# Performance work log

Measured on AMD Instinct MI355X. Metric: run time of the kernel, lower is better.

The kernel has to match this reference:

```python
import jax, jax.numpy as jnp
import numpy as np

N = 8192
F_IN = 512
F_OUT = 64
ALPHA = 0.2  # LeakyReLU negative slope
NEG_INF = -9e15


def setup_inputs() -> dict:
    key = jax.random.key(0)
    k1, k2, k3, k4 = jax.random.split(key, 4)
    inp = jax.random.normal(k1, (N, F_IN), dtype=jnp.float32)
    adj = jax.random.randint(k2, (N, N), 0, 2, dtype=jnp.int32)
    W = jax.random.normal(k3, (F_IN, F_OUT), dtype=jnp.float32) * 0.05
    a = jax.random.normal(k4, (2 * F_OUT, 1), dtype=jnp.float32) * 0.05
    return {"inp": inp, "adj": adj, "W": W, "a": a}


def reference(inp, adj, W, a):
    # h = W(inp): [N, F_OUT]
    h = inp @ W
    # a([h_i || h_j]) decomposes exactly into a1.h_i + a2.h_j, avoiding the
    # [N*N, 2F] concat tensor while computing identical math.
    f1 = h @ a[:F_OUT]        # [N, 1] source-node term
    f2 = h @ a[F_OUT:]        # [N, 1] target-node term
    e = jax.nn.leaky_relu(f1 + f2.T, negative_slope=ALPHA)  # [N, N]
    masked = jnp.where(adj > 0, e, jnp.float32(NEG_INF))
    attention = jax.nn.softmax(masked, axis=1)  # dropout is no-op at inference
    h_prime = attention @ h   # [N, F_OUT]
    return jax.nn.elu(h_prime)  # concat=True branch
```

## Files before the change

kernel.cpp:

```cpp
#include <hip/hip_runtime.h>

#define NN   8192
#define FIN  512
#define FOUT 64

typedef __attribute__((ext_vector_type(8))) short short8;
typedef __attribute__((ext_vector_type(4))) float floatx4;

__device__ __forceinline__ unsigned f2bf_u(float f) {
  union { float f; unsigned u; } v; v.f = f;
  return (v.u + 0x7fffu + ((v.u >> 16) & 1u)) >> 16;
}
__device__ __forceinline__ unsigned pack2(float a, float b) {
  return f2bf_u(a) | (f2bf_u(b) << 16);
}

__global__ __launch_bounds__(256) void k1_gemm_h(
    const float* __restrict__ inp, const float* __restrict__ W,
    const float* __restrict__ a,
    float* __restrict__ f1, float* __restrict__ f2,
    unsigned short* __restrict__ hT)
{
  __shared__ unsigned short at[32][72];
  __shared__ unsigned short wt[64][72];
  __shared__ float hsm[32][65];
  __shared__ float alds[2 * FOUT];

  const int tid   = threadIdx.x;
  const int rbase = blockIdx.x * 32;
  if (tid < 2 * FOUT) alds[tid] = a[tid];

  const int lane = tid & 63;
  const int wv   = tid >> 6;
  const int l15  = lane & 15;
  const int q    = lane >> 4;
  const int mi   = wv & 1;
  const int ni0  = (wv >> 1) * 2;

  const int r_a  = tid >> 3;
  const int k8   = (tid & 7) * 8;
  const int n_w  = tid & 63;
  const int kb_w = (tid >> 6) * 16;

  floatx4 acc0 = {0.f, 0.f, 0.f, 0.f};
  floatx4 acc1 = {0.f, 0.f, 0.f, 0.f};

  for (int kk0 = 0; kk0 < FIN; kk0 += 64) {
    __syncthreads();
    const float* ap = inp + (rbase + r_a) * FIN + kk0 + k8;
    float4 v0 = *(const float4*)ap;
    float4 v1 = *(const float4*)(ap + 4);
    *(uint4*)&at[r_a][k8] = make_uint4(pack2(v0.x, v0.y), pack2(v0.z, v0.w),
                                       pack2(v1.x, v1.y), pack2(v1.z, v1.w));
#pragma unroll
    for (int kk2 = 0; kk2 < 16; ++kk2)
      wt[n_w][kb_w + kk2] = (unsigned short)f2bf_u(W[(kk0 + kb_w + kk2) * FOUT + n_w]);
    __syncthreads();
#pragma unroll
    for (int ks = 0; ks < 2; ++ks) {
      short8 af = *(const short8*)&at[mi * 16 + l15][ks * 32 + q * 8];
      short8 b0 = *(const short8*)&wt[ni0 * 16 + l15][ks * 32 + q * 8];
      short8 b1 = *(const short8*)&wt[(ni0 + 1) * 16 + l15][ks * 32 + q * 8];
      acc0 = __builtin_amdgcn_mfma_f32_16x16x32_bf16(af, b0, acc0, 0, 0, 0);
      acc1 = __builtin_amdgcn_mfma_f32_16x16x32_bf16(af, b1, acc1, 0, 0, 0);
    }
  }

  {
    const int m0 = mi * 16 + q * 4;
    const int i0 = rbase + m0;
    {
      const int n = ni0 * 16 + l15;
#pragma unroll
      for (int rg = 0; rg < 4; ++rg) hsm[m0 + rg][n] = acc0[rg];
      *(uint2*)&hT[n * NN + i0] = make_uint2(pack2(acc0[0], acc0[1]),
                                             pack2(acc0[2], acc0[3]));
    }
    {
      const int n = (ni0 + 1) * 16 + l15;
#pragma unroll
      for (int rg = 0; rg < 4; ++rg) hsm[m0 + rg][n] = acc1[rg];
      *(uint2*)&hT[n * NN + i0] = make_uint2(pack2(acc1[0], acc1[1]),
                                             pack2(acc1[2], acc1[3]));
    }
  }
  __syncthreads();
  if (tid < 32) {
    float s1 = 0.f, s2 = 0.f;
#pragma unroll 8
    for (int c = 0; c < FOUT; ++c) {
      float hv = hsm[tid][c];
      s1 += hv * alds[c];
      s2 += hv * alds[FOUT + c];
    }
    f1[rbase + tid] = s1;
    f2[rbase + tid] = s2;
  }
}

__global__ __launch_bounds__(256) void k2_attn(
    const int* __restrict__ adj,
    const float* __restrict__ f1g, const float* __restrict__ f2g,
    const unsigned short* __restrict__ hT,
    float* __restrict__ out)
{
  __shared__ unsigned short wlds[16][136];
  __shared__ unsigned short hlds[64][136];
  __shared__ float lred[16][17];
  __shared__ float linv_s[16];

  const int tid   = threadIdx.x;
  const int rbase = blockIdx.x * 16;
  const int lane  = tid & 63;
  const int wv    = tid >> 6;
  const int l15   = lane & 15;
  const int q     = lane >> 4;

  const int r  = tid >> 4;
  const int c8 = (tid & 15) * 8;
  const float f1v = f1g[rbase + r];
  const int* arow = adj + (size_t)(rbase + r) * NN + c8;

  const int fh = tid >> 2;
  const int sg = (tid & 3) * 32;
  const unsigned short* hrow = hT + (size_t)fh * NN + sg;

  floatx4 acc = {0.f, 0.f, 0.f, 0.f};
  float lsum = 0.f;

  int4 A0, A1; float4 F0, F1; int4 H0, H1, H2, H3;
  A0 = *(const int4*)(arow);
  A1 = *(const int4*)(arow + 4);
  F0 = *(const float4*)(f2g + c8);
  F1 = *(const float4*)(f2g + c8 + 4);
  H0 = *(const int4*)(hrow);
  H1 = *(const int4*)(hrow + 8);
  H2 = *(const int4*)(hrow + 16);
  H3 = *(const int4*)(hrow + 24);

  for (int it = 0; it < 64; ++it) {
    __syncthreads();
    float e, w0, w1, w2, w3, w4, w5, w6, w7;
    e = f1v + F0.x; e = (e > 0.f) ? e : 0.2f * e; w0 = A0.x ? __expf(e) : 0.f;
    e = f1v + F0.y; e = (e > 0.f) ? e : 0.2f * e; w1 = A0.y ? __expf(e) : 0.f;
    e = f1v + F0.z; e = (e > 0.f) ? e : 0.2f * e; w2 = A0.z ? __expf(e) : 0.f;
    e = f1v + F0.w; e = (e > 0.f) ? e : 0.2f * e; w3 = A0.w ? __expf(e) : 0.f;
    e = f1v + F1.x; e = (e > 0.f) ? e : 0.2f * e; w4 = A1.x ? __expf(e) : 0.f;
    e = f1v + F1.y; e = (e > 0.f) ? e : 0.2f * e; w5 = A1.y ? __expf(e) : 0.f;
    e = f1v + F1.z; e = (e > 0.f) ? e : 0.2f * e; w6 = A1.z ? __expf(e) : 0.f;
    e = f1v + F1.w; e = (e > 0.f) ? e : 0.2f * e; w7 = A1.w ? __expf(e) : 0.f;
    lsum += ((w0 + w1) + (w2 + w3)) + ((w4 + w5) + (w6 + w7));
    *(uint4*)&wlds[r][c8] = make_uint4(pack2(w0, w1), pack2(w2, w3),
                                       pack2(w4, w5), pack2(w6, w7));
    *(int4*)&hlds[fh][sg]      = H0;
    *(int4*)&hlds[fh][sg + 8]  = H1;
    *(int4*)&hlds[fh][sg + 16] = H2;
    *(int4*)&hlds[fh][sg + 24] = H3;
    __syncthreads();
    if (it < 63) {
      const int kk = (it + 1) * 128;
      A0 = *(const int4*)(arow + kk);
      A1 = *(const int4*)(arow + kk + 4);
      F0 = *(const float4*)(f2g + kk + c8);
      F1 = *(const float4*)(f2g + kk + c8 + 4);
      H0 = *(const int4*)(hrow + kk);
      H1 = *(const int4*)(hrow + kk + 8);
      H2 = *(const int4*)(hrow + kk + 16);
      H3 = *(const int4*)(hrow + kk + 24);
    }
#pragma unroll
    for (int ks = 0; ks < 4; ++ks) {
      short8 af = *(const short8*)&wlds[l15][ks * 32 + q * 8];
      short8 bf = *(const short8*)&hlds[wv * 16 + l15][ks * 32 + q * 8];
      acc = __builtin_amdgcn_mfma_f32_16x16x32_bf16(af, bf, acc, 0, 0, 0);
    }
  }

  lred[r][tid & 15] = lsum;
  __syncthreads();
  if (tid < 16) {
    float s = 0.f;
#pragma unroll
    for (int i = 0; i < 16; ++i) s += lred[tid][i];
    linv_s[tid] = 1.f / s;
  }
  __syncthreads();

  const int m0  = q * 4;
  const int nn2 = wv * 16 + l15;
#pragma unroll
  for (int rg = 0; rg < 4; ++rg) {
    float v = acc[rg] * linv_s[m0 + rg];
    v = (v > 0.f) ? v : (__expf(v) - 1.f);
    out[(size_t)(rbase + m0 + rg) * FOUT + nn2] = v;
  }
}

extern "C" void kernel_launch(void* const* d_in, const int* in_sizes, int n_in,
                              void* d_out, int out_size, void* d_ws, size_t ws_size,
                              hipStream_t stream) {
  (void)in_sizes; (void)n_in; (void)out_size; (void)ws_size;
  const float* inp = (const float*)d_in[0];
  const int*   adj = (const int*)d_in[1];
  const float* W   = (const float*)d_in[2];
  const float* a   = (const float*)d_in[3];
  float* out = (float*)d_out;

  float* f1 = (float*)d_ws;
  float* f2 = f1 + NN;
  unsigned short* hT = (unsigned short*)(f2 + NN);

  k1_gemm_h<<<NN / 32, 256, 0, stream>>>(inp, W, a, f1, f2, hT);
  k2_attn<<<NN / 16, 256, 0, stream>>>(adj, f1, f2, hT, out);
}
```

Measured before the change: 387.1 us.

## Split attention K dimension, use 32x32 MFMA from registers, add combine kernel

Rewrites the attention kernel so each block handles 32 rows over half of the neighbor dimension. Each wave computes attention weights in registers and feeds them straight into 32x32x16 bf16 MFMAs with h loaded directly from global, which drops the per-iteration LDS staging and barriers. Partial sums and row normalizers go to workspace and are merged by a new combine kernel that also applies the softmax normalization and ELU. The trade is an extra launch plus the partial-buffer traffic, paid for more parallelism and less synchronization. The pass over the 256 MB int32 adjacency stays the dominant cost.

```diff
diff --git a/kernel.cpp b/kernel.cpp
--- a/kernel.cpp
+++ b/kernel.cpp
@@ -3,9 +3,11 @@
 #define NN   8192
 #define FIN  512
 #define FOUT 64
-
-typedef __attribute__((ext_vector_type(8))) short short8;
-typedef __attribute__((ext_vector_type(4))) float floatx4;
+#define KHALF 4096
+
+typedef __attribute__((ext_vector_type(8)))  short short8;
+typedef __attribute__((ext_vector_type(4)))  float floatx4;
+typedef __attribute__((ext_vector_type(16))) float floatx16;
 
 __device__ __forceinline__ unsigned f2bf_u(float f) {
   union { float f; unsigned u; } v; v.f = f;
@@ -13,6 +15,9 @@
 }
 __device__ __forceinline__ unsigned pack2(float a, float b) {
   return f2bf_u(a) | (f2bf_u(b) << 16);
+}
+__device__ __forceinline__ short8 as_s8(int4 v) {
+  union { int4 a; short8 b; } u; u.a = v; return u.b;
 }
 
 __global__ __launch_bounds__(256) void k1_gemm_h(
@@ -98,102 +103,125 @@
   }
 }
 
-__global__ __launch_bounds__(256) void k2_attn(
+__device__ __forceinline__ short8 mkw(const int4 A0, const int4 A1,
+                                      const float4 F0, const float4 F1,
+                                      const float f1v, float& lsum) {
+  float e, w0, w1, w2, w3, w4, w5, w6, w7;
+  e = f1v + F0.x; e = fmaxf(e, 0.2f * e); w0 = A0.x ? __expf(e) : 0.f;
+  e = f1v + F0.y; e = fmaxf(e, 0.2f * e); w1 = A0.y ? __expf(e) : 0.f;
+  e = f1v + F0.z; e = fmaxf(e, 0.2f * e); w2 = A0.z ? __expf(e) : 0.f;
+  e = f1v + F0.w; e = fmaxf(e, 0.2f * e); w3 = A0.w ? __expf(e) : 0.f;
+  e = f1v + F1.x; e = fmaxf(e, 0.2f * e); w4 = A1.x ? __expf(e) : 0.f;
+  e = f1v + F1.y; e = fmaxf(e, 0.2f * e); w5 = A1.y ? __expf(e) : 0.f;
+  e = f1v + F1.z; e = fmaxf(e, 0.2f * e); w6 = A1.z ? __expf(e) : 0.f;
+  e = f1v + F1.w; e = fmaxf(e, 0.2f * e); w7 = A1.w ? __expf(e) : 0.f;
+  lsum += ((w0 + w1) + (w2 + w3)) + ((w4 + w5) + (w6 + w7));
+  uint4 u = make_uint4(pack2(w0, w1), pack2(w2, w3), pack2(w4, w5), pack2(w6, w7));
+  union { uint4 a; short8 b; } c; c.a = u; return c.b;
+}
+
+__global__ __launch_bounds__(256, 2) void k2_attn(
     const int* __restrict__ adj,
     const float* __restrict__ f1g, const float* __restrict__ f2g,
     const unsigned short* __restrict__ hT,
+    float* __restrict__ part, float* __restrict__ lpart)
+{
+  __shared__ float pbuf[4][2048];
+  __shared__ float lsw[4][32];
+
+  const int tid   = threadIdx.x;
+  const int wv    = tid >> 6;
+  const int lane  = tid & 63;
+  const int i32   = lane & 31;
+  const int hi    = lane >> 5;
+  const int rbase = (blockIdx.x >> 1) * 32;
+  const int kh    = blockIdx.x & 1;
+  const int kbase = kh * KHALF + wv * 32 + hi * 8;
+
+  const int*            ap  = adj + (size_t)(rbase + i32) * NN + kbase;
+  const float*          fp  = f2g + kbase;
+  const unsigned short* h0p = hT + (size_t)i32 * NN + kbase;
+  const unsigned short* h1p = h0p + (size_t)32 * NN;
+  const float f1v = f1g[rbase + i32];
+
+  floatx16 acc0 = {0,0,0,0,0,0,0,0,0,0,0,0,0,0,0,0};
+  floatx16 acc1 = {0,0,0,0,0,0,0,0,0,0,0,0,0,0,0,0};
+  float lsum = 0.f;
+
+  int4  A0  = *(const int4*)(ap);       int4  A1  = *(const int4*)(ap + 4);
+  int4  A2  = *(const int4*)(ap + 16);  int4  A3  = *(const int4*)(ap + 20);
+  float4 F0 = *(const float4*)(fp);     float4 F1 = *(const float4*)(fp + 4);
+  float4 F2 = *(const float4*)(fp + 16);float4 F3 = *(const float4*)(fp + 20);
+  int4  H00 = *(const int4*)(h0p);      int4  H01 = *(const int4*)(h0p + 16);
+  int4  H10 = *(const int4*)(h1p);      int4  H11 = *(const int4*)(h1p + 16);
+
+  for (int it = 0; it < KHALF / 128; ++it) {
+    const int nk = (it < KHALF / 128 - 1) ? (it + 1) * 128 : 0;
+    int4  nA0 = *(const int4*)(ap + nk);       int4  nA1 = *(const int4*)(ap + nk + 4);
+    int4  nA2 = *(const int4*)(ap + nk + 16);  int4  nA3 = *(const int4*)(ap + nk + 20);
+    float4 nF0 = *(const float4*)(fp + nk);    float4 nF1 = *(const float4*)(fp + nk + 4);
+    float4 nF2 = *(const float4*)(fp + nk + 16);float4 nF3 = *(const float4*)(fp + nk + 20);
+    int4  nH00 = *(const int4*)(h0p + nk);     int4  nH01 = *(const int4*)(h0p + nk + 16);
+    int4  nH10 = *(const int4*)(h1p + nk);     int4  nH11 = *(const int4*)(h1p + nk + 16);
+
+    short8 b0 = mkw(A0, A1, F0, F1, f1v, lsum);
+    acc0 = __builtin_amdgcn_mfma_f32_32x32x16_bf16(as_s8(H00), b0, acc0, 0, 0, 0);
+    acc1 = __builtin_amdgcn_mfma_f32_32x32x16_bf16(as_s8(H10), b0, acc1, 0, 0, 0);
+    short8 b1 = mkw(A2, A3, F2, F3, f1v, lsum);
+    acc0 = __builtin_amdgcn_mfma_f32_32x32x16_bf16(as_s8(H01), b1, acc0, 0, 0, 0);
+    acc1 = __builtin_amdgcn_mfma_f32_32x32x16_bf16(as_s8(H11), b1, acc1, 0, 0, 0);
+
+    A0 = nA0; A1 = nA1; A2 = nA2; A3 = nA3;
+    F0 = nF0; F1 = nF1; F2 = nF2; F3 = nF3;
+    H00 = nH00; H01 = nH01; H10 = nH10; H11 = nH11;
+  }
+
+  lsum += __shfl_xor(lsum, 32, 64);
+  if (lane < 32) lsw[wv][i32] = lsum;
+
+#pragma unroll
+  for (int rg = 0; rg < 16; ++rg) {
+    const int m = (rg & 3) + 8 * (rg >> 2) + 4 * hi;
+    pbuf[wv][i32 * 64 + m]      = acc0[rg];
+    pbuf[wv][i32 * 64 + 32 + m] = acc1[rg];
+  }
+  __syncthreads();
+
+  const int e0 = tid * 8;
+  const int irow = rbase + (e0 >> 6);
+  const int f0c  = e0 & 63;
+  float* dst = part + ((size_t)kh * NN + irow) * 64 + f0c;
+#pragma unroll
+  for (int c = 0; c < 2; ++c) {
+    float4 s = *(const float4*)&pbuf[0][e0 + c * 4];
+    float4 s1 = *(const float4*)&pbuf[1][e0 + c * 4];
+    float4 s2 = *(const float4*)&pbuf[2][e0 + c * 4];
+    float4 s3 = *(const float4*)&pbuf[3][e0 + c * 4];
+    s.x += s1.x + s2.x + s3.x; s.y += s1.y + s2.y + s3.y;
+    s.z += s1.z + s2.z + s3.z; s.w += s1.w + s2.w + s3.w;
+    *(float4*)(dst + c * 4) = s;
+  }
+  if (tid < 32)
+    lpart[(size_t)kh * NN + rbase + tid] =
+        lsw[0][tid] + lsw[1][tid] + lsw[2][tid] + lsw[3][tid];
+}
+
+__global__ __launch_bounds__(256) void k3_combine(
+    const float* __restrict__ part, const float* __restrict__ lpart,
     float* __restrict__ out)
 {
-  __shared__ unsigned short wlds[16][136];
-  __shared__ unsigned short hlds[64][136];
-  __shared__ float lred[16][17];
-  __shared__ float linv_s[16];
-
-  const int tid   = threadIdx.x;
-  const int rbase = blockIdx.x * 16;
-  const int lane  = tid & 63;
-  const int wv    = tid >> 6;
-  const int l15   = lane & 15;
-  const int q     = lane >> 4;
-
-  const int r  = tid >> 4;
-  const int c8 = (tid & 15) * 8;
-  const float f1v = f1g[rbase + r];
-  const int* arow = adj + (size_t)(rbase + r) * NN + c8;
-
-  const int fh = tid >> 2;
-  const int sg = (tid & 3) * 32;
-  const unsigned short* hrow = hT + (size_t)fh * NN + sg;
-
-  floatx4 acc = {0.f, 0.f, 0.f, 0.f};
-  float lsum = 0.f;
-
-  int4 A0, A1; float4 F0, F1; int4 H0, H1, H2, H3;
-  A0 = *(const int4*)(arow);
-  A1 = *(const int4*)(arow + 4);
-  F0 = *(const float4*)(f2g + c8);
-  F1 = *(const float4*)(f2g + c8 + 4);
-  H0 = *(const int4*)(hrow);
-  H1 = *(const int4*)(hrow + 8);
-  H2 = *(const int4*)(hrow + 16);
-  H3 = *(const int4*)(hrow + 24);
-
-  for (int it = 0; it < 64; ++it) {
-    __syncthreads();
-    float e, w0, w1, w2, w3, w4, w5, w6, w7;
-    e = f1v + F0.x; e = (e > 0.f) ? e : 0.2f * e; w0 = A0.x ? __expf(e) : 0.f;
-    e = f1v + F0.y; e = (e > 0.f) ? e : 0.2f * e; w1 = A0.y ? __expf(e) : 0.f;
-    e = f1v + F0.z; e = (e > 0.f) ? e : 0.2f * e; w2 = A0.z ? __expf(e) : 0.f;
-    e = f1v + F0.w; e = (e > 0.f) ? e : 0.2f * e; w3 = A0.w ? __expf(e) : 0.f;
-    e = f1v + F1.x; e = (e > 0.f) ? e : 0.2f * e; w4 = A1.x ? __expf(e) : 0.f;
-    e = f1v + F1.y; e = (e > 0.f) ? e : 0.2f * e; w5 = A1.y ? __expf(e) : 0.f;
-    e = f1v + F1.z; e = (e > 0.f) ? e : 0.2f * e; w6 = A1.z ? __expf(e) : 0.f;
-    e = f1v + F1.w; e = (e > 0.f) ? e : 0.2f * e; w7 = A1.w ? __expf(e) : 0.f;
-    lsum += ((w0 + w1) + (w2 + w3)) + ((w4 + w5) + (w6 + w7));
-    *(uint4*)&wlds[r][c8] = make_uint4(pack2(w0, w1), pack2(w2, w3),
-                                       pack2(w4, w5), pack2(w6, w7));
-    *(int4*)&hlds[fh][sg]      = H0;
-    *(int4*)&hlds[fh][sg + 8]  = H1;
-    *(int4*)&hlds[fh][sg + 16] = H2;
-    *(int4*)&hlds[fh][sg + 24] = H3;
-    __syncthreads();
-    if (it < 63) {
-      const int kk = (it + 1) * 128;
-      A0 = *(const int4*)(arow + kk);
-      A1 = *(const int4*)(arow + kk + 4);
-      F0 = *(const float4*)(f2g + kk + c8);
-      F1 = *(const float4*)(f2g + kk + c8 + 4);
-      H0 = *(const int4*)(hrow + kk);
-      H1 = *(const int4*)(hrow + kk + 8);
-      H2 = *(const int4*)(hrow + kk + 16);
-      H3 = *(const int4*)(hrow + kk + 24);
-    }
-#pragma unroll
-    for (int ks = 0; ks < 4; ++ks) {
-      short8 af = *(const short8*)&wlds[l15][ks * 32 + q * 8];
-      short8 bf = *(const short8*)&hlds[wv * 16 + l15][ks * 32 + q * 8];
-      acc = __builtin_amdgcn_mfma_f32_16x16x32_bf16(af, bf, acc, 0, 0, 0);
-    }
-  }
-
-  lred[r][tid & 15] = lsum;
-  __syncthreads();
-  if (tid < 16) {
-    float s = 0.f;
-#pragma unroll
-    for (int i = 0; i < 16; ++i) s += lred[tid][i];
-    linv_s[tid] = 1.f / s;
-  }
-  __syncthreads();
-
-  const int m0  = q * 4;
-  const int nn2 = wv * 16 + l15;
-#pragma unroll
-  for (int rg = 0; rg < 4; ++rg) {
-    float v = acc[rg] * linv_s[m0 + rg];
-    v = (v > 0.f) ? v : (__expf(v) - 1.f);
-    out[(size_t)(rbase + m0 + rg) * FOUT + nn2] = v;
-  }
+  const int gid = blockIdx.x * 256 + threadIdx.x;
+  const int i = gid >> 4;
+  const int c = (gid & 15) * 4;
+  const float inv = 1.f / (lpart[i] + lpart[NN + i]);
+  float4 p0 = *(const float4*)(part + (size_t)i * 64 + c);
+  float4 p1 = *(const float4*)(part + ((size_t)NN + i) * 64 + c);
+  float4 v;
+  v.x = (p0.x + p1.x) * inv; v.x = (v.x > 0.f) ? v.x : (__expf(v.x) - 1.f);
+  v.y = (p0.y + p1.y) * inv; v.y = (v.y > 0.f) ? v.y : (__expf(v.y) - 1.f);
+  v.z = (p0.z + p1.z) * inv; v.z = (v.z > 0.f) ? v.z : (__expf(v.z) - 1.f);
+  v.w = (p0.w + p1.w) * inv; v.w = (v.w > 0.f) ? v.w : (__expf(v.w) - 1.f);
+  *(float4*)(out + (size_t)i * 64 + c) = v;
 }
 
 extern "C" void kernel_launch(void* const* d_in, const int* in_sizes, int n_in,
@@ -209,7 +237,10 @@
   float* f1 = (float*)d_ws;
   float* f2 = f1 + NN;
   unsigned short* hT = (unsigned short*)(f2 + NN);
+  float* part  = (float*)(hT + (size_t)FOUT * NN);
+  float* lpart = part + 2 * (size_t)NN * FOUT;
 
   k1_gemm_h<<<NN / 32, 256, 0, stream>>>(inp, W, a, f1, f2, hT);
-  k2_attn<<<NN / 16, 256, 0, stream>>>(adj, f1, f2, hT, out);
-}
+  k2_attn<<<(NN / 32) * 2, 256, 0, stream>>>(adj, f1, f2, hT, part, lpart);
+  k3_combine<<<NN * FOUT / 4 / 256, 256, 0, stream>>>(part, lpart, out);
+}
```

Measured after the change: 399.7 us. 1.03x slower.
